# Performance work log

Measured on AMD Instinct MI355X. Metric: run time of the kernel, lower is better.

## Reference

```python
import jax, jax.numpy as jnp
import numpy as np

B, S, H, T, DI, HID, K, HEADS = 8, 1024, 768, 8, 64, 128, 8, 2
NEG = 1.0e12


def _build_adj(spans):
    # spans: [K,3] int; returns [K+1,K+1] edge multiplicity matrix (dst, src)
    s, e = spans[:, 0], spans[:, 1]
    same = (s[:, None] == s[None, :]) & (e[:, None] == e[None, :])
    # contain[i,j]: span i strictly contains span j (source appends this edge twice)
    contain = (s[:, None] <= s[None, :]) & (e[None, :] <= e[:, None]) & (~same)
    N = K + 1
    adj = jnp.eye(N, dtype=jnp.float32)                    # PyG add_self_loops
    adj = adj.at[1:, 0].add(1.0)                           # global -> span i
    adj = adj.at[0, 1:].add(1.0)                           # span i -> global
    adj = adj.at[1:, 1:].add(2.0 * contain.T.astype(jnp.float32))
    return adj


def _gat(x, adj, W, a_src, a_dst, b):
    # x [N,F]; adj [N,N] multiplicity with layout (dst, src). PyG GATConv math.
    N = x.shape[0]
    h = (x @ W).reshape(N, HEADS, -1)                      # [N,Hd,D]
    asrc = jnp.einsum('nhd,hd->nh', h, a_src)
    adst = jnp.einsum('nhd,hd->nh', h, a_dst)
    ee = jax.nn.leaky_relu(adst[:, None, :] + asrc[None, :, :], 0.2)  # [dst,src,Hd]
    logmult = jnp.where(adj > 0, jnp.log(jnp.maximum(adj, 1e-20)), 0.0)
    scores = jnp.where(adj[:, :, None] > 0, ee + logmult[:, :, None], -1e30)
    attn = jax.nn.softmax(scores, axis=1)                  # softmax over source nodes
    out = jnp.einsum('dsh,shf->dhf', attn, h).reshape(N, -1)
    return out + b


def _layernorm(x, g, bta):
    mu = x.mean(-1, keepdims=True)
    var = x.var(-1, keepdims=True)
    return (x - mu) / jnp.sqrt(var + 1e-5) * g + bta


def _forward(hidden, attention_mask, spans, W1, a_src1, a_dst1, b1, ln_g, ln_b,
             W2, a_src2, a_dst2, b2, dense_W, dense_b,
             g_centers, g_sigmas, g_weights, corr):
    start, end, etype = spans[..., 0], spans[..., 1], spans[..., 2]  # [B,K]
    pos = jnp.arange(S)
    span_mask = ((pos[None, None, :] >= start[..., None]) &
                 (pos[None, None, :] <= end[..., None])).astype(hidden.dtype)  # [B,K,S]
    span_len = (end - start + 1).astype(hidden.dtype)
    span_feat = jnp.einsum('bks,bsh->bkh', span_mask, hidden) / span_len[..., None]
    global_feat = hidden.mean(axis=1, keepdims=True)                 # [B,1,H]
    nodes = jnp.concatenate([global_feat, span_feat], axis=1)        # [B,K+1,H]
    adj = jax.vmap(_build_adj)(spans)                                # [B,K+1,K+1]

    g1 = jax.vmap(lambda x, a: _gat(x, a, W1, a_src1, a_dst1, b1))(nodes, adj)
    g1 = _layernorm(jax.nn.relu(g1), ln_g, ln_b)
    g2 = jax.vmap(lambda x, a: _gat(x, a, W2, a_src2, a_dst2, b2))(g1, adj)
    g2 = jax.nn.relu(g2)
    enhanced = g2.mean(axis=1)                                       # per-graph mean pool [B,2*HID]

    cover = span_mask.sum(axis=1)                                    # [B,S] how many spans cover token s
    token_enh = cover[..., None] * enhanced[:, None, :]              # [B,S,2*HID]
    combined = jnp.concatenate([hidden, token_enh], axis=-1)

    qk = (combined @ dense_W + dense_b).reshape(B, S, T, 2 * DI)
    qw, kw = qk[..., :DI], qk[..., DI:]

    # RoPE (sin/cos interleaved exactly as in source)
    inv = jnp.power(10000.0, -2.0 * jnp.arange(DI // 2) / DI)
    ang = pos[:, None].astype(jnp.float32) * inv[None, :]            # [S,DI/2]
    sin = jnp.repeat(jnp.sin(ang), 2, axis=-1)[None, :, None, :]     # [1,S,1,DI]
    cos = jnp.repeat(jnp.cos(ang), 2, axis=-1)[None, :, None, :]

    def rot(v):
        v2 = jnp.stack([-v[..., 1::2], v[..., ::2]], axis=-1).reshape(v.shape)
        return v * cos + v2 * sin

    qw, kw = rot(qw), rot(kw)

    logits = jnp.einsum('bmtd,bntd->btmn', qw, kw)                   # [B,T,S,S]

    # multi-modal gaussian kernel span maps (vectorized over batch/span/component)
    pf = pos.astype(jnp.float32)
    dxs = pf[None, None, None, :] - start[..., None, None] - g_centers[None, None, :, None]
    dxe = pf[None, None, None, :] - end[..., None, None] - g_centers[None, None, :, None]
    Ksr = g_weights[None, None, :, None] * jnp.exp(-0.5 * (dxs / g_sigmas[None, None, :, None]) ** 2)
    Ken = g_weights[None, None, :, None] * jnp.exp(-0.5 * (dxe / g_sigmas[None, None, :, None]) ** 2)
    gmap = jnp.einsum('bkcm,bkcn->bkmn', Ksr, Ken)                   # [B,K,S,S]
    corr_span = corr[etype]                                          # [B,K,T]
    logits = logits + jnp.einsum('bkt,bkmn->btmn', corr_span, gmap)

    pad = attention_mask[:, None, None, :]                           # key-dim-only mask (as in source)
    logits = logits * pad - (1.0 - pad) * NEG
    tril = jnp.tril(jnp.ones((S, S), logits.dtype), -1)
    logits = logits - tril * NEG
    return logits / jnp.sqrt(jnp.float32(DI))


def setup_inputs() -> dict:
    key = jax.random.key(0)
    ks = jax.random.split(key, 16)
    hidden = jax.random.normal(ks[0], (B, S, H), jnp.float32)
    attention_mask = jnp.ones((B, S), jnp.float32)
    start = jax.random.randint(ks[1], (B, K), 0, S - 32)
    length = jax.random.randint(ks[2], (B, K), 1, 16)
    spans = jnp.stack([start, start + length,
                       jax.random.randint(ks[3], (B, K), 0, T)], axis=-1).astype(jnp.int32)
    sd = 0.05
    return {
        'hidden': hidden,
        'attention_mask': attention_mask,
        'spans': spans,
        'W1': jax.random.normal(ks[4], (H, HEADS * HID), jnp.float32) * sd,
        'a_src1': jax.random.normal(ks[5], (HEADS, HID), jnp.float32) * sd,
        'a_dst1': jax.random.normal(ks[6], (HEADS, HID), jnp.float32) * sd,
        'b1': jnp.zeros((HEADS * HID,), jnp.float32),
        'ln_g': jnp.ones((HEADS * HID,), jnp.float32),
        'ln_b': jnp.zeros((HEADS * HID,), jnp.float32),
        'W2': jax.random.normal(ks[7], (HEADS * HID, HEADS * HID), jnp.float32) * sd,
        'a_src2': jax.random.normal(ks[8], (HEADS, HID), jnp.float32) * sd,
        'a_dst2': jax.random.normal(ks[9], (HEADS, HID), jnp.float32) * sd,
        'b2': jnp.zeros((HEADS * HID,), jnp.float32),
        'dense_W': jax.random.normal(ks[10], (H + HEADS * HID, T * 2 * DI), jnp.float32) * sd,
        'dense_b': jnp.zeros((T * 2 * DI,), jnp.float32),
        'g_centers': jnp.array([0.0, 0.0], jnp.float32),
        'g_sigmas': jnp.array([1.0, 3.0], jnp.float32),
        'g_weights': jnp.array([0.5, 0.5], jnp.float32),
        'corr': jnp.eye(T, dtype=jnp.float32),
    }


def reference(hidden, attention_mask, spans, W1, a_src1, a_dst1, b1, ln_g, ln_b,
              W2, a_src2, a_dst2, b2, dense_W, dense_b,
              g_centers, g_sigmas, g_weights, corr):
    return _forward(hidden, attention_mask, spans, W1, a_src1, a_dst1, b1, ln_g, ln_b,
                    W2, a_src2, a_dst2, b2, dense_W, dense_b,
                    g_centers, g_sigmas, g_weights, corr)
```

## Files before the change

### kernel.cpp

```cpp
#include <hip/hip_runtime.h>
#include <cstdint>
#include <cstddef>

#define BB 8
#define SS 1024
#define HH 768
#define TT 8
#define DII 64
#define HIDD 128
#define KSP 8
#define NHEADS 2
#define NNODES 9
#define GDIM 256
#define CDIM 1024
#define DAUGP 96
#define NEGV 1e12f

using bf16x8 = __attribute__((ext_vector_type(8))) __bf16;
using f32x4  = __attribute__((ext_vector_type(4))) float;

static __device__ inline unsigned short f2bf(float x) {
  union { float f; unsigned u; } v; v.f = x;
  unsigned r = v.u + 0x7fff + ((v.u >> 16) & 1);
  return (unsigned short)(r >> 16);
}

__global__ void kc1_cvt_hidden(const float* __restrict__ hidden, unsigned short* __restrict__ hbf) {
  int idx = blockIdx.x * 256 + threadIdx.x;
  float4 v = *(const float4*)(hidden + (size_t)idx * 4);
  ushort4 o; o.x = f2bf(v.x); o.y = f2bf(v.y); o.z = f2bf(v.z); o.w = f2bf(v.w);
  *(ushort4*)(hbf + (size_t)idx * 4) = o;
}

__global__ void kc2_cvt_wtop(const float* __restrict__ dense_W, unsigned short* __restrict__ WtopT) {
  __shared__ float t[32][33];
  int k0 = blockIdx.x * 32, n0 = blockIdx.y * 32;
  int tid = threadIdx.x;
  int r = tid >> 3, c4 = (tid & 7) * 4;
  float4 v = *(const float4*)&dense_W[(size_t)(k0 + r) * CDIM + n0 + c4];
  t[r][c4 + 0] = v.x; t[r][c4 + 1] = v.y; t[r][c4 + 2] = v.z; t[r][c4 + 3] = v.w;
  __syncthreads();
  int ro = tid >> 3, co4 = (tid & 7) * 4;
  ushort4 o;
  o.x = f2bf(t[co4 + 0][ro]); o.y = f2bf(t[co4 + 1][ro]);
  o.z = f2bf(t[co4 + 2][ro]); o.w = f2bf(t[co4 + 3][ro]);
  *(ushort4*)&WtopT[(size_t)(n0 + ro) * HH + k0 + co4] = o;
}

__global__ void k1a_spans(const float* __restrict__ hidden, const int* __restrict__ spans,
                          float* __restrict__ nodes, float* __restrict__ cover) {
  int b = blockIdx.x, tid = threadIdx.x;
  __shared__ int sp[KSP * 3];
  if (tid < KSP * 3) sp[tid] = spans[b * KSP * 3 + tid];
  __syncthreads();
  for (int s = tid; s < SS; s += 256) {
    float c = 0.f;
    #pragma unroll
    for (int k = 0; k < KSP; k++)
      c += (s >= sp[k * 3] && s <= sp[k * 3 + 1]) ? 1.f : 0.f;
    cover[b * SS + s] = c;
  }
  const float* hb = hidden + (size_t)b * SS * HH;
  for (int k = 0; k < KSP; k++) {
    int st = sp[k * 3], en = sp[k * 3 + 1];
    float inv = 1.f / (float)(en - st + 1);
    #pragma unroll
    for (int ci = 0; ci < 3; ci++) {
      int c = tid + ci * 256;
      float a = 0.f;
      #pragma unroll
      for (int j = 0; j < 16; j++) {
        int s = st + j;
        int sc = (s <= en) ? s : en;
        float v = hb[(size_t)sc * HH + c];
        a += (s <= en) ? v : 0.f;
      }
      nodes[((size_t)b * NNODES + (k + 1)) * HH + c] = a * inv;
    }
  }
}

__global__ void k1b_partial(const float* __restrict__ hidden, float* __restrict__ part) {
  int z = blockIdx.x, b = blockIdx.y, tid = threadIdx.x;
  const float* hb = hidden + (size_t)b * SS * HH;
  #pragma unroll
  for (int j = 0; j < 3; j++) {
    int c = tid + j * 256;
    float acc = 0.f;
    #pragma unroll 8
    for (int r = z * 64; r < z * 64 + 64; r++) acc += hb[(size_t)r * HH + c];
    part[((size_t)b * 16 + z) * HH + c] = acc;
  }
}
__global__ void k1c_reduce(const float* __restrict__ part, float* __restrict__ nodes) {
  int b = blockIdx.x, tid = threadIdx.x;
  #pragma unroll
  for (int j = 0; j < 3; j++) {
    int c = tid + j * 256;
    float s = 0.f;
    #pragma unroll
    for (int z = 0; z < 16; z++) s += part[((size_t)b * 16 + z) * HH + c];
    nodes[(size_t)b * NNODES * HH + c] = s / (float)SS;
  }
}

__global__ __launch_bounds__(256) void k2_gat(
    const float* __restrict__ nodes_g, const int* __restrict__ spans,
    const float* __restrict__ W1, const float* __restrict__ a_src1,
    const float* __restrict__ a_dst1, const float* __restrict__ b1,
    const float* __restrict__ ln_g, const float* __restrict__ ln_b,
    const float* __restrict__ W2, const float* __restrict__ a_src2,
    const float* __restrict__ a_dst2, const float* __restrict__ b2,
    float* __restrict__ enhg) {
  int b = blockIdx.x, tid = threadIdx.x;
  __shared__ __align__(16) float nod[NNODES * HH];
  __shared__ __align__(16) float hbuf[NNODES * GDIM];
  __shared__ __align__(16) float gbuf[NNODES * GDIM];
  __shared__ float asrc[NNODES * NHEADS], adst[NNODES * NHEADS];
  __shared__ float adjm[NNODES * NNODES];
  __shared__ float attn[NNODES * NNODES * NHEADS];
  __shared__ float mu_s[NNODES], rs_s[NNODES];
  __shared__ int sp[KSP * 3];
  if (tid < KSP * 3) sp[tid] = spans[b * KSP * 3 + tid];
  for (int i = tid; i < NNODES * HH; i += 256)
    nod[i] = nodes_g[(size_t)b * NNODES * HH + i];
  __syncthreads();
  {
    float acc[NNODES];
    #pragma unroll
    for (int n = 0; n < NNODES; n++) acc[n] = 0.f;
    #pragma unroll 2
    for (int d0 = 0; d0 < HH; d0 += 4) {
      float4 nv[NNODES];
      #pragma unroll
      for (int n = 0; n < NNODES; n++) nv[n] = *(const float4*)&nod[n * HH + d0];
      float w0 = W1[(size_t)(d0 + 0) * GDIM + tid];
      float w1 = W1[(size_t)(d0 + 1) * GDIM + tid];
      float w2 = W1[(size_t)(d0 + 2) * GDIM + tid];
      float w3 = W1[(size_t)(d0 + 3) * GDIM + tid];
      #pragma unroll
      for (int n = 0; n < NNODES; n++)
        acc[n] += nv[n].x * w0 + nv[n].y * w1 + nv[n].z * w2 + nv[n].w * w3;
    }
    #pragma unroll
    for (int n = 0; n < NNODES; n++) hbuf[n * GDIM + tid] = acc[n];
  }
  if (tid < NNODES * NNODES) {
    int i = tid / NNODES, j = tid % NNODES;
    float a = (i == j) ? 1.f : 0.f;
    if (i > 0 && j == 0) a += 1.f;
    if (i == 0 && j > 0) a += 1.f;
    if (i > 0 && j > 0 && i != j) {
      int x = j - 1, y = i - 1;
      int sx = sp[x * 3], ex = sp[x * 3 + 1], sy = sp[y * 3], ey = sp[y * 3 + 1];
      bool same = (sx == sy) && (ex == ey);
      if (sx <= sy && ey <= ex && !same) a += 2.f;
    }
    adjm[tid] = a;
  }
  __syncthreads();
  if (tid < NNODES * NHEADS) {
    int n = tid >> 1, hd = tid & 1;
    float sa = 0.f, sd = 0.f;
    #pragma unroll 8
    for (int f = 0; f < HIDD; f++) {
      float v = hbuf[n * GDIM + hd * HIDD + f];
      sa += v * a_src1[hd * HIDD + f];
      sd += v * a_dst1[hd * HIDD + f];
    }
    asrc[tid] = sa; adst[tid] = sd;
  }
  __syncthreads();
  if (tid < NNODES * NHEADS) {
    int d = tid >> 1, hd = tid & 1;
    float sc[NNODES]; float mx = -1e30f;
    for (int s2 = 0; s2 < NNODES; s2++) {
      float a = adjm[d * NNODES + s2]; float v;
      if (a > 0.f) {
        float e = adst[d * 2 + hd] + asrc[s2 * 2 + hd];
        e = (e > 0.f) ? e : 0.2f * e;
        v = e + __logf(a);
      } else v = -1e30f;
      sc[s2] = v; mx = fmaxf(mx, v);
    }
    float ssum = 0.f;
    for (int s2 = 0; s2 < NNODES; s2++) { float ex = __expf(sc[s2] - mx); sc[s2] = ex; ssum += ex; }
    float inv = 1.f / ssum;
    for (int s2 = 0; s2 < NNODES; s2++) attn[(d * NNODES + s2) * NHEADS + hd] = sc[s2] * inv;
  }
  __syncthreads();
  {
    int hd = tid >> 7;
    float bb = b1[tid];
    for (int d = 0; d < NNODES; d++) {
      float acc = bb;
      #pragma unroll
      for (int s2 = 0; s2 < NNODES; s2++)
        acc += attn[(d * NNODES + s2) * NHEADS + hd] * hbuf[s2 * GDIM + tid];
      gbuf[d * GDIM + tid] = fmaxf(acc, 0.f);
    }
  }
  __syncthreads();
  if (tid < NNODES) {
    float s1 = 0.f, s2v = 0.f;
    #pragma unroll 8
    for (int o = 0; o < GDIM; o++) { float v = gbuf[tid * GDIM + o]; s1 += v; s2v += v * v; }
    float mu = s1 / (float)GDIM;
    float var = s2v / (float)GDIM - mu * mu;
    mu_s[tid] = mu; rs_s[tid] = rsqrtf(var + 1e-5f);
  }
  __syncthreads();
  {
    float g = ln_g[tid], bt = ln_b[tid];
    for (int d = 0; d < NNODES; d++)
      gbuf[d * GDIM + tid] = (gbuf[d * GDIM + tid] - mu_s[d]) * rs_s[d] * g + bt;
  }
  __syncthreads();
  {
    float acc[NNODES];
    #pragma unroll
    for (int n = 0; n < NNODES; n++) acc[n] = 0.f;
    #pragma unroll 2
    for (int d0 = 0; d0 < GDIM; d0 += 4) {
      float4 nv[NNODES];
      #pragma unroll
      for (int n = 0; n < NNODES; n++) nv[n] = *(const float4*)&gbuf[n * GDIM + d0];
      float w0 = W2[(size_t)(d0 + 0) * GDIM + tid];
      float w1 = W2[(size_t)(d0 + 1) * GDIM + tid];
      float w2 = W2[(size_t)(d0 + 2) * GDIM + tid];
      float w3 = W2[(size_t)(d0 + 3) * GDIM + tid];
      #pragma unroll
      for (int n = 0; n < NNODES; n++)
        acc[n] += nv[n].x * w0 + nv[n].y * w1 + nv[n].z * w2 + nv[n].w * w3;
    }
    #pragma unroll
    for (int n = 0; n < NNODES; n++) hbuf[n * GDIM + tid] = acc[n];
  }
  __syncthreads();
  if (tid < NNODES * NHEADS) {
    int n = tid >> 1, hd = tid & 1;
    float sa = 0.f, sd = 0.f;
    #pragma unroll 8
    for (int f = 0; f < HIDD; f++) {
      float v = hbuf[n * GDIM + hd * HIDD + f];
      sa += v * a_src2[hd * HIDD + f];
      sd += v * a_dst2[hd * HIDD + f];
    }
    asrc[tid] = sa; adst[tid] = sd;
  }
  __syncthreads();
  if (tid < NNODES * NHEADS) {
    int d = tid >> 1, hd = tid & 1;
    float sc[NNODES]; float mx = -1e30f;
    for (int s2 = 0; s2 < NNODES; s2++) {
      float a = adjm[d * NNODES + s2]; float v;
      if (a > 0.f) {
        float e = adst[d * 2 + hd] + asrc[s2 * 2 + hd];
        e = (e > 0.f) ? e : 0.2f * e;
        v = e + __logf(a);
      } else v = -1e30f;
      sc[s2] = v; mx = fmaxf(mx, v);
    }
    float ssum = 0.f;
    for (int s2 = 0; s2 < NNODES; s2++) { float ex = __expf(sc[s2] - mx); sc[s2] = ex; ssum += ex; }
    float inv = 1.f / ssum;
    for (int s2 = 0; s2 < NNODES; s2++) attn[(d * NNODES + s2) * NHEADS + hd] = sc[s2] * inv;
  }
  __syncthreads();
  {
    int hd = tid >> 7;
    float bb = b2[tid];
    float msum = 0.f;
    for (int d = 0; d < NNODES; d++) {
      float acc = bb;
      #pragma unroll
      for (int s2 = 0; s2 < NNODES; s2++)
        acc += attn[(d * NNODES + s2) * NHEADS + hd] * hbuf[s2 * GDIM + tid];
      msum += fmaxf(acc, 0.f);
    }
    enhg[b * GDIM + tid] = msum / 9.f;
  }
}

__global__ void k2b_e2(const float* __restrict__ enhg, const float* __restrict__ dense_W,
                       float* __restrict__ E2) {
  int b = blockIdx.y, tid = threadIdx.x;
  int o = blockIdx.x * 256 + tid;
  __shared__ __align__(16) float eh[GDIM];
  eh[tid] = enhg[b * GDIM + tid];
  __syncthreads();
  float acc = 0.f;
  #pragma unroll 2
  for (int d = 0; d < GDIM; d += 4) {
    float4 ev = *(const float4*)&eh[d];
    acc += ev.x * dense_W[(size_t)(HH + d + 0) * CDIM + o];
    acc += ev.y * dense_W[(size_t)(HH + d + 1) * CDIM + o];
    acc += ev.z * dense_W[(size_t)(HH + d + 2) * CDIM + o];
    acc += ev.w * dense_W[(size_t)(HH + d + 3) * CDIM + o];
  }
  E2[b * CDIM + o] = acc;
}

__global__ __launch_bounds__(256) void k3_dense(
    const unsigned short* __restrict__ hbf, const unsigned short* __restrict__ WtopT,
    const float* __restrict__ dense_b, const float* __restrict__ cover,
    const float* __restrict__ E2, float* __restrict__ qk) {
  __shared__ unsigned short As[128 * 40];
  __shared__ unsigned short Bs[128 * 40];
  int tid = threadIdx.x;
  int n0 = blockIdx.x * 128, m0 = blockIdx.y * 128;
  int wave = tid >> 6, lane = tid & 63;
  int wr = wave >> 1, wc = wave & 1;
  int colL = lane & 15, quad = lane >> 4;
  f32x4 acc[4][4];
  #pragma unroll
  for (int i = 0; i < 4; i++)
    #pragma unroll
    for (int j = 0; j < 4; j++) { acc[i][j][0] = 0.f; acc[i][j][1] = 0.f; acc[i][j][2] = 0.f; acc[i][j][3] = 0.f; }
  for (int k0 = 0; k0 < HH; k0 += 32) {
    uint4 va[2], vb[2];
    #pragma unroll
    for (int it = 0; it < 2; it++) {
      int idx = tid + it * 256;
      int r = idx >> 2, seg = idx & 3;
      va[it] = *(const uint4*)(hbf + (size_t)(m0 + r) * HH + k0 + seg * 8);
      vb[it] = *(const uint4*)(WtopT + (size_t)(n0 + r) * HH + k0 + seg * 8);
    }
    __syncthreads();
    #pragma unroll
    for (int it = 0; it < 2; it++) {
      int idx = tid + it * 256;
      int r = idx >> 2, seg = idx & 3;
      *(uint4*)&As[r * 40 + seg * 8] = va[it];
      *(uint4*)&Bs[r * 40 + seg * 8] = vb[it];
    }
    __syncthreads();
    bf16x8 af[4], bf[4];
    #pragma unroll
    for (int tm = 0; tm < 4; tm++)
      af[tm] = *(const bf16x8*)&As[(wr * 64 + tm * 16 + colL) * 40 + quad * 8];
    #pragma unroll
    for (int tn = 0; tn < 4; tn++)
      bf[tn] = *(const bf16x8*)&Bs[(wc * 64 + tn * 16 + colL) * 40 + quad * 8];
    #pragma unroll
    for (int tm = 0; tm < 4; tm++)
      #pragma unroll
      for (int tn = 0; tn < 4; tn++)
        acc[tm][tn] = __builtin_amdgcn_mfma_f32_16x16x32_bf16(af[tm], bf[tn], acc[tm][tn], 0, 0, 0);
  }
  int b = m0 >> 10;
  #pragma unroll
  for (int tn = 0; tn < 4; tn++) {
    int col = n0 + wc * 64 + tn * 16 + colL;
    float e2 = E2[b * CDIM + col];
    float db = dense_b[col];
    #pragma unroll
    for (int tm = 0; tm < 4; tm++) {
      int rbase = m0 + wr * 64 + tm * 16 + quad * 4;
      #pragma unroll
      for (int r = 0; r < 4; r++) {
        int m = rbase + r;
        qk[(size_t)m * CDIM + col] = acc[tm][tn][r] + cover[m] * e2 + db;
      }
    }
  }
}

__global__ void k4_ropeaug(const float* __restrict__ qk, const int* __restrict__ spans,
                           const float* __restrict__ corr, const float* __restrict__ gc,
                           const float* __restrict__ gs, const float* __restrict__ gw,
                           unsigned short* __restrict__ Qa, unsigned short* __restrict__ Ka) {
  int tid = threadIdx.x;
  int g = tid >> 5, lane = tid & 31;
  int row = blockIdx.x * 8 + g;
  int b = row >> 10, s = row & 1023;
  const float* qrow = qk + (size_t)row * CDIM;
  const float LOG1E4_32 = 0.28782313662425576f;
  #pragma unroll
  for (int it = 0; it < 8; it++) {
    int cbase = it * 128 + lane * 4;
    float4 v = *(const float4*)(qrow + cbase);
    int t = cbase >> 7;
    int d = cbase & 127;
    int dd = d & 63;
    int i0 = dd >> 1;
    float inv0 = __expf(-(float)i0 * LOG1E4_32);
    float inv1 = __expf(-(float)(i0 + 1) * LOG1E4_32);
    float s0, c0, s1, c1;
    __sincosf((float)s * inv0, &s0, &c0);
    __sincosf((float)s * inv1, &s1, &c1);
    float o0 = v.x * c0 - v.y * s0;
    float o1 = v.y * c0 + v.x * s0;
    float o2 = v.z * c1 - v.w * s1;
    float o3 = v.w * c1 + v.z * s1;
    ushort4 w; w.x = f2bf(o0); w.y = f2bf(o1); w.z = f2bf(o2); w.w = f2bf(o3);
    size_t base = ((size_t)(b * TT + t) * SS + s) * DAUGP;
    if (d < 64) *(ushort4*)(Qa + base + dd) = w;
    else        *(ushort4*)(Ka + base + dd) = w;
  }
  int j = lane & 15;
  int kp = j >> 1, c = j & 1;
  int st = spans[(b * KSP + kp) * 3 + 0];
  int en = spans[(b * KSP + kp) * 3 + 1];
  int et = spans[(b * KSP + kp) * 3 + 2];
  float sig = gs[c], wgt = gw[c], ce = gc[c];
  if (lane < 16) {
    float dx = ((float)(s - st) - ce) / sig;
    float e = wgt * __expf(-0.5f * dx * dx);
    #pragma unroll
    for (int t = 0; t < TT; t++) {
      size_t base = ((size_t)(b * TT + t) * SS + s) * DAUGP;
      Qa[base + 64 + j] = f2bf(corr[et * TT + t] * e);
      Qa[base + 80 + j] = 0;
    }
  } else {
    float dx = ((float)(s - en) - ce) / sig;
    unsigned short bv = f2bf(wgt * __expf(-0.5f * dx * dx));
    #pragma unroll
    for (int t = 0; t < TT; t++) {
      size_t base = ((size_t)(b * TT + t) * SS + s) * DAUGP;
      Ka[base + 64 + j] = bv;
      Ka[base + 80 + j] = 0;
    }
  }
}

__global__ __launch_bounds__(256) void k5_logits(
    const unsigned short* __restrict__ Qa, const unsigned short* __restrict__ Ka,
    const float* __restrict__ amask, float* __restrict__ out) {
  int bz = blockIdx.z; int b = bz >> 3;
  int n0 = blockIdx.x * 128, m0 = blockIdx.y * 128;
  int tid = threadIdx.x;
  if (n0 + 127 < m0) {
    int r0 = tid >> 5, c4 = (tid & 31) * 4;
    float4 pv = *(const float4*)&amask[b * SS + n0 + c4];
    float4 o;
    o.x = (-(1.f - pv.x) * NEGV - NEGV) * 0.125f;
    o.y = (-(1.f - pv.y) * NEGV - NEGV) * 0.125f;
    o.z = (-(1.f - pv.z) * NEGV - NEGV) * 0.125f;
    o.w = (-(1.f - pv.w) * NEGV - NEGV) * 0.125f;
    for (int r = r0; r < 128; r += 8)
      *(float4*)&out[((size_t)bz * SS + m0 + r) * SS + n0 + c4] = o;
    return;
  }
  __shared__ unsigned short Qs[128 * 104];
  __shared__ unsigned short Ks[128 * 104];
  const unsigned short* Qrow = Qa + ((size_t)bz * SS + m0) * DAUGP;
  const unsigned short* Krow = Ka + ((size_t)bz * SS + n0) * DAUGP;
  #pragma unroll
  for (int it = 0; it < 6; it++) {
    int idx = tid + it * 256;
    int r = idx / 12, seg = idx % 12;
    uint4 vq = *(const uint4*)(Qrow + (size_t)r * DAUGP + seg * 8);
    uint4 vk = *(const uint4*)(Krow + (size_t)r * DAUGP + seg * 8);
    *(uint4*)&Qs[r * 104 + seg * 8] = vq;
    *(uint4*)&Ks[r * 104 + seg * 8] = vk;
  }
  __syncthreads();
  int wave = tid >> 6, lane = tid & 63;
  int wr = wave >> 1, wc = wave & 1;
  int colL = lane & 15, quad = lane >> 4;
  f32x4 acc[4][4];
  #pragma unroll
  for (int i = 0; i < 4; i++)
    #pragma unroll
    for (int j = 0; j < 4; j++) { acc[i][j][0] = 0.f; acc[i][j][1] = 0.f; acc[i][j][2] = 0.f; acc[i][j][3] = 0.f; }
  #pragma unroll
  for (int ks = 0; ks < 3; ks++) {
    bf16x8 af[4], bf[4];
    #pragma unroll
    for (int tm = 0; tm < 4; tm++)
      af[tm] = *(const bf16x8*)&Qs[(wr * 64 + tm * 16 + colL) * 104 + ks * 32 + quad * 8];
    #pragma unroll
    for (int tn = 0; tn < 4; tn++)
      bf[tn] = *(const bf16x8*)&Ks[(wc * 64 + tn * 16 + colL) * 104 + ks * 32 + quad * 8];
    #pragma unroll
    for (int tm = 0; tm < 4; tm++)
      #pragma unroll
      for (int tn = 0; tn < 4; tn++)
        acc[tm][tn] = __builtin_amdgcn_mfma_f32_16x16x32_bf16(af[tm], bf[tn], acc[tm][tn], 0, 0, 0);
  }
  #pragma unroll
  for (int tn = 0; tn < 4; tn++) {
    int col = n0 + wc * 64 + tn * 16 + colL;
    float p = amask[b * SS + col];
    float negp = -(1.f - p) * NEGV;
    #pragma unroll
    for (int tm = 0; tm < 4; tm++) {
      int rbase = m0 + wr * 64 + tm * 16 + quad * 4;
      #pragma unroll
      for (int r = 0; r < 4; r++) {
        int m = rbase + r;
        float v = acc[tm][tn][r] * p + negp;
        if (col < m) v -= NEGV;
        out[((size_t)bz * SS + m) * SS + col] = v * 0.125f;
      }
    }
  }
}

extern "C" void kernel_launch(void* const* d_in, const int* in_sizes, int n_in,
                              void* d_out, int out_size, void* d_ws, size_t ws_size,
                              hipStream_t stream) {
  const float* hidden  = (const float*)d_in[0];
  const float* amask   = (const float*)d_in[1];
  const int*   spans   = (const int*)d_in[2];
  const float* W1      = (const float*)d_in[3];
  const float* a_src1  = (const float*)d_in[4];
  const float* a_dst1  = (const float*)d_in[5];
  const float* b1      = (const float*)d_in[6];
  const float* ln_g    = (const float*)d_in[7];
  const float* ln_b    = (const float*)d_in[8];
  const float* W2      = (const float*)d_in[9];
  const float* a_src2  = (const float*)d_in[10];
  const float* a_dst2  = (const float*)d_in[11];
  const float* b2      = (const float*)d_in[12];
  const float* dense_W = (const float*)d_in[13];
  const float* dense_b = (const float*)d_in[14];
  const float* gc      = (const float*)d_in[15];
  const float* gs      = (const float*)d_in[16];
  const float* gw      = (const float*)d_in[17];
  const float* corr    = (const float*)d_in[18];

  char* wsb = (char*)d_ws;
  float* qk            = (float*)wsb;                         wsb += (size_t)BB * SS * CDIM * 4;
  unsigned short* hbf  = (unsigned short*)wsb;                wsb += (size_t)BB * SS * HH * 2;
  unsigned short* WtopT= (unsigned short*)wsb;                wsb += (size_t)CDIM * HH * 2;
  unsigned short* Qa   = (unsigned short*)wsb;                wsb += (size_t)BB * TT * SS * DAUGP * 2;
  unsigned short* Ka   = (unsigned short*)wsb;                wsb += (size_t)BB * TT * SS * DAUGP * 2;
  float* nodes         = (float*)wsb;                         wsb += (size_t)BB * NNODES * HH * 4;
  float* cover         = (float*)wsb;                         wsb += (size_t)BB * SS * 4;
  float* E2            = (float*)wsb;                         wsb += (size_t)BB * CDIM * 4;
  float* enhg          = (float*)wsb;                         wsb += (size_t)BB * GDIM * 4;
  float* part          = (float*)wsb;                         wsb += (size_t)BB * 16 * HH * 4;
  float* outp = (float*)d_out;

  kc1_cvt_hidden<<<(BB * SS * HH / 4) / 256, 256, 0, stream>>>(hidden, hbf);
  kc2_cvt_wtop<<<dim3(HH / 32, CDIM / 32), 256, 0, stream>>>(dense_W, WtopT);
  k1a_spans<<<BB, 256, 0, stream>>>(hidden, spans, nodes, cover);
  k1b_partial<<<dim3(16, BB), 256, 0, stream>>>(hidden, part);
  k1c_reduce<<<BB, 256, 0, stream>>>(part, nodes);
  k2_gat<<<BB, 256, 0, stream>>>(nodes, spans, W1, a_src1, a_dst1, b1, ln_g, ln_b,
                                 W2, a_src2, a_dst2, b2, enhg);
  k2b_e2<<<dim3(CDIM / 256, BB), 256, 0, stream>>>(enhg, dense_W, E2);
  k3_dense<<<dim3(CDIM / 128, (BB * SS) / 128), 256, 0, stream>>>(hbf, WtopT, dense_b,
                                                                  cover, E2, qk);
  k4_ropeaug<<<(BB * SS) / 8, 256, 0, stream>>>(qk, spans, corr, gc, gs, gw, Qa, Ka);
  k5_logits<<<dim3(8, 8, BB * TT), 256, 0, stream>>>(Qa, Ka, amask, outp);
}
```

Before: 598.4 us.

## Fuse RoPE into dense GEMM epilogue, merge conversion with mean partials, widen GAT

The rotary embedding is now applied in the dense GEMM epilogue, using a lane shuffle to fetch the paired element, and bf16 results are written straight into Qa/Ka. This removes the fp32 qk intermediate and its round trip through global memory. The hidden-to-bf16 conversion now also produces the partial sums for the global mean, so hidden is read once less, and the final reduce is folded into the GAT kernel. The span pooling runs on a per-span grid, and the GAT kernel uses 512 threads that split the K dimension of each matmul. Risks include scattered 2-byte epilogue stores and the extra shared-memory reduction step in the GAT kernel.

```diff
diff --git a/kernel.cpp b/kernel.cpp
--- a/kernel.cpp
+++ b/kernel.cpp
@@ -25,11 +25,24 @@
   return (unsigned short)(r >> 16);
 }
 
-__global__ void kc1_cvt_hidden(const float* __restrict__ hidden, unsigned short* __restrict__ hbf) {
-  int idx = blockIdx.x * 256 + threadIdx.x;
-  float4 v = *(const float4*)(hidden + (size_t)idx * 4);
-  ushort4 o; o.x = f2bf(v.x); o.y = f2bf(v.y); o.z = f2bf(v.z); o.w = f2bf(v.w);
-  *(ushort4*)(hbf + (size_t)idx * 4) = o;
+__global__ void kc1b_cvt_partial(const float* __restrict__ hidden,
+                                 unsigned short* __restrict__ hbf,
+                                 float* __restrict__ part) {
+  int z = blockIdx.x, b = blockIdx.y, tid = threadIdx.x;
+  const float* hb = hidden + (size_t)b * SS * HH;
+  unsigned short* ho = hbf + (size_t)b * SS * HH;
+  #pragma unroll
+  for (int j = 0; j < 3; j++) {
+    int c = tid + j * 256;
+    float acc = 0.f;
+    #pragma unroll 8
+    for (int r = z * 64; r < z * 64 + 64; r++) {
+      float v = hb[(size_t)r * HH + c];
+      ho[(size_t)r * HH + c] = f2bf(v);
+      acc += v;
+    }
+    part[((size_t)b * 16 + z) * HH + c] = acc;
+  }
 }
 
 __global__ void kc2_cvt_wtop(const float* __restrict__ dense_W, unsigned short* __restrict__ WtopT) {
@@ -49,63 +62,39 @@
 
 __global__ void k1a_spans(const float* __restrict__ hidden, const int* __restrict__ spans,
                           float* __restrict__ nodes, float* __restrict__ cover) {
-  int b = blockIdx.x, tid = threadIdx.x;
+  int k = blockIdx.x, b = blockIdx.y, tid = threadIdx.x;
   __shared__ int sp[KSP * 3];
   if (tid < KSP * 3) sp[tid] = spans[b * KSP * 3 + tid];
   __syncthreads();
-  for (int s = tid; s < SS; s += 256) {
+  if (tid < 128) {
+    int s = k * 128 + tid;
     float c = 0.f;
     #pragma unroll
-    for (int k = 0; k < KSP; k++)
-      c += (s >= sp[k * 3] && s <= sp[k * 3 + 1]) ? 1.f : 0.f;
+    for (int kk = 0; kk < KSP; kk++)
+      c += (s >= sp[kk * 3] && s <= sp[kk * 3 + 1]) ? 1.f : 0.f;
     cover[b * SS + s] = c;
   }
+  int st = sp[k * 3], en = sp[k * 3 + 1];
+  float inv = 1.f / (float)(en - st + 1);
   const float* hb = hidden + (size_t)b * SS * HH;
-  for (int k = 0; k < KSP; k++) {
-    int st = sp[k * 3], en = sp[k * 3 + 1];
-    float inv = 1.f / (float)(en - st + 1);
-    #pragma unroll
-    for (int ci = 0; ci < 3; ci++) {
-      int c = tid + ci * 256;
-      float a = 0.f;
-      #pragma unroll
-      for (int j = 0; j < 16; j++) {
-        int s = st + j;
-        int sc = (s <= en) ? s : en;
-        float v = hb[(size_t)sc * HH + c];
-        a += (s <= en) ? v : 0.f;
-      }
-      nodes[((size_t)b * NNODES + (k + 1)) * HH + c] = a * inv;
-    }
-  }
-}
-
-__global__ void k1b_partial(const float* __restrict__ hidden, float* __restrict__ part) {
-  int z = blockIdx.x, b = blockIdx.y, tid = threadIdx.x;
-  const float* hb = hidden + (size_t)b * SS * HH;
-  #pragma unroll
-  for (int j = 0; j < 3; j++) {
-    int c = tid + j * 256;
-    float acc = 0.f;
-    #pragma unroll 8
-    for (int r = z * 64; r < z * 64 + 64; r++) acc += hb[(size_t)r * HH + c];
-    part[((size_t)b * 16 + z) * HH + c] = acc;
-  }
-}
-__global__ void k1c_reduce(const float* __restrict__ part, float* __restrict__ nodes) {
-  int b = blockIdx.x, tid = threadIdx.x;
-  #pragma unroll
-  for (int j = 0; j < 3; j++) {
-    int c = tid + j * 256;
-    float s = 0.f;
-    #pragma unroll
-    for (int z = 0; z < 16; z++) s += part[((size_t)b * 16 + z) * HH + c];
-    nodes[(size_t)b * NNODES * HH + c] = s / (float)SS;
-  }
-}
-
-__global__ __launch_bounds__(256) void k2_gat(
-    const float* __restrict__ nodes_g, const int* __restrict__ spans,
+  #pragma unroll
+  for (int ci = 0; ci < 3; ci++) {
+    int c = tid + ci * 256;
+    float a = 0.f;
+    #pragma unroll
+    for (int j = 0; j < 16; j++) {
+      int s = st + j;
+      int sc = (s <= en) ? s : en;
+      float v = hb[(size_t)sc * HH + c];
+      a += (s <= en) ? v : 0.f;
+    }
+    nodes[((size_t)b * NNODES + (k + 1)) * HH + c] = a * inv;
+  }
+}
+
+__global__ __launch_bounds__(512) void k2_gat(
+    const float* __restrict__ part, const float* __restrict__ nodes_g,
+    const int* __restrict__ spans,
     const float* __restrict__ W1, const float* __restrict__ a_src1,
     const float* __restrict__ a_dst1, const float* __restrict__ b1,
     const float* __restrict__ ln_g, const float* __restrict__ ln_b,
@@ -116,37 +105,52 @@
   __shared__ __align__(16) float nod[NNODES * HH];
   __shared__ __align__(16) float hbuf[NNODES * GDIM];
   __shared__ __align__(16) float gbuf[NNODES * GDIM];
+  __shared__ __align__(16) float pbuf[2 * NNODES * GDIM];
   __shared__ float asrc[NNODES * NHEADS], adst[NNODES * NHEADS];
   __shared__ float adjm[NNODES * NNODES];
   __shared__ float attn[NNODES * NNODES * NHEADS];
   __shared__ float mu_s[NNODES], rs_s[NNODES];
   __shared__ int sp[KSP * 3];
   if (tid < KSP * 3) sp[tid] = spans[b * KSP * 3 + tid];
-  for (int i = tid; i < NNODES * HH; i += 256)
-    nod[i] = nodes_g[(size_t)b * NNODES * HH + i];
+  for (int c = tid; c < HH; c += 512) {
+    float s = 0.f;
+    #pragma unroll
+    for (int z = 0; z < 16; z++) s += part[((size_t)b * 16 + z) * HH + c];
+    nod[c] = s * (1.f / (float)SS);
+  }
+  for (int i = tid; i < (NNODES - 1) * HH; i += 512)
+    nod[HH + i] = nodes_g[(size_t)b * NNODES * HH + HH + i];
   __syncthreads();
   {
+    int col = tid & 255, h = tid >> 8;
     float acc[NNODES];
     #pragma unroll
     for (int n = 0; n < NNODES; n++) acc[n] = 0.f;
+    int dlo = h * 384;
     #pragma unroll 2
-    for (int d0 = 0; d0 < HH; d0 += 4) {
+    for (int d0 = dlo; d0 < dlo + 384; d0 += 4) {
       float4 nv[NNODES];
       #pragma unroll
       for (int n = 0; n < NNODES; n++) nv[n] = *(const float4*)&nod[n * HH + d0];
-      float w0 = W1[(size_t)(d0 + 0) * GDIM + tid];
-      float w1 = W1[(size_t)(d0 + 1) * GDIM + tid];
-      float w2 = W1[(size_t)(d0 + 2) * GDIM + tid];
-      float w3 = W1[(size_t)(d0 + 3) * GDIM + tid];
+      float w0 = W1[(size_t)(d0 + 0) * GDIM + col];
+      float w1 = W1[(size_t)(d0 + 1) * GDIM + col];
+      float w2 = W1[(size_t)(d0 + 2) * GDIM + col];
+      float w3 = W1[(size_t)(d0 + 3) * GDIM + col];
       #pragma unroll
       for (int n = 0; n < NNODES; n++)
         acc[n] += nv[n].x * w0 + nv[n].y * w1 + nv[n].z * w2 + nv[n].w * w3;
     }
     #pragma unroll
-    for (int n = 0; n < NNODES; n++) hbuf[n * GDIM + tid] = acc[n];
-  }
-  if (tid < NNODES * NNODES) {
-    int i = tid / NNODES, j = tid % NNODES;
+    for (int n = 0; n < NNODES; n++) pbuf[(h * NNODES + n) * GDIM + col] = acc[n];
+  }
+  __syncthreads();
+  if (tid < GDIM) {
+    #pragma unroll
+    for (int n = 0; n < NNODES; n++)
+      hbuf[n * GDIM + tid] = pbuf[n * GDIM + tid] + pbuf[(NNODES + n) * GDIM + tid];
+  } else if (tid < 256 + NNODES * NNODES) {
+    int q = tid - 256;
+    int i = q / NNODES, j = q % NNODES;
     float a = (i == j) ? 1.f : 0.f;
     if (i > 0 && j == 0) a += 1.f;
     if (i == 0 && j > 0) a += 1.f;
@@ -156,7 +160,7 @@
       bool same = (sx == sy) && (ex == ey);
       if (sx <= sy && ey <= ex && !same) a += 2.f;
     }
-    adjm[tid] = a;
+    adjm[q] = a;
   }
   __syncthreads();
   if (tid < NNODES * NHEADS) {
@@ -189,11 +193,11 @@
     for (int s2 = 0; s2 < NNODES; s2++) attn[(d * NNODES + s2) * NHEADS + hd] = sc[s2] * inv;
   }
   __syncthreads();
-  {
+  if (tid < 256) {
     int hd = tid >> 7;
-    float bb = b1[tid];
+    float bbv = b1[tid];
     for (int d = 0; d < NNODES; d++) {
-      float acc = bb;
+      float acc = bbv;
       #pragma unroll
       for (int s2 = 0; s2 < NNODES; s2++)
         acc += attn[(d * NNODES + s2) * NHEADS + hd] * hbuf[s2 * GDIM + tid];
@@ -210,31 +214,39 @@
     mu_s[tid] = mu; rs_s[tid] = rsqrtf(var + 1e-5f);
   }
   __syncthreads();
-  {
+  if (tid < 256) {
     float g = ln_g[tid], bt = ln_b[tid];
     for (int d = 0; d < NNODES; d++)
       gbuf[d * GDIM + tid] = (gbuf[d * GDIM + tid] - mu_s[d]) * rs_s[d] * g + bt;
   }
   __syncthreads();
   {
+    int col = tid & 255, h = tid >> 8;
     float acc[NNODES];
     #pragma unroll
     for (int n = 0; n < NNODES; n++) acc[n] = 0.f;
+    int dlo = h * 128;
     #pragma unroll 2
-    for (int d0 = 0; d0 < GDIM; d0 += 4) {
+    for (int d0 = dlo; d0 < dlo + 128; d0 += 4) {
       float4 nv[NNODES];
       #pragma unroll
       for (int n = 0; n < NNODES; n++) nv[n] = *(const float4*)&gbuf[n * GDIM + d0];
-      float w0 = W2[(size_t)(d0 + 0) * GDIM + tid];
-      float w1 = W2[(size_t)(d0 + 1) * GDIM + tid];
-      float w2 = W2[(size_t)(d0 + 2) * GDIM + tid];
-      float w3 = W2[(size_t)(d0 + 3) * GDIM + tid];
+      float w0 = W2[(size_t)(d0 + 0) * GDIM + col];
+      float w1 = W2[(size_t)(d0 + 1) * GDIM + col];
+      float w2 = W2[(size_t)(d0 + 2) * GDIM + col];
+      float w3 = W2[(size_t)(d0 + 3) * GDIM + col];
       #pragma unroll
       for (int n = 0; n < NNODES; n++)
         acc[n] += nv[n].x * w0 + nv[n].y * w1 + nv[n].z * w2 + nv[n].w * w3;
     }
     #pragma unroll
-    for (int n = 0; n < NNODES; n++) hbuf[n * GDIM + tid] = acc[n];
+    for (int n = 0; n < NNODES; n++) pbuf[(h * NNODES + n) * GDIM + col] = acc[n];
+  }
+  __syncthreads();
+  if (tid < GDIM) {
+    #pragma unroll
+    for (int n = 0; n < NNODES; n++)
+      hbuf[n * GDIM + tid] = pbuf[n * GDIM + tid] + pbuf[(NNODES + n) * GDIM + tid];
   }
   __syncthreads();
   if (tid < NNODES * NHEADS) {
@@ -267,12 +279,12 @@
     for (int s2 = 0; s2 < NNODES; s2++) attn[(d * NNODES + s2) * NHEADS + hd] = sc[s2] * inv;
   }
   __syncthreads();
-  {
+  if (tid < 256) {
     int hd = tid >> 7;
-    float bb = b2[tid];
+    float bbv = b2[tid];
     float msum = 0.f;
     for (int d = 0; d < NNODES; d++) {
-      float acc = bb;
+      float acc = bbv;
       #pragma unroll
       for (int s2 = 0; s2 < NNODES; s2++)
         acc += attn[(d * NNODES + s2) * NHEADS + hd] * hbuf[s2 * GDIM + tid];
@@ -304,7 +316,8 @@
 __global__ __launch_bounds__(256) void k3_dense(
     const unsigned short* __restrict__ hbf, const unsigned short* __restrict__ WtopT,
     const float* __restrict__ dense_b, const float* __restrict__ cover,
-    const float* __restrict__ E2, float* __restrict__ qk) {
+    const float* __restrict__ E2,
+    unsigned short* __restrict__ Qa, unsigned short* __restrict__ Ka) {
   __shared__ unsigned short As[128 * 40];
   __shared__ unsigned short Bs[128 * 40];
   int tid = threadIdx.x;
@@ -349,55 +362,45 @@
         acc[tm][tn] = __builtin_amdgcn_mfma_f32_16x16x32_bf16(af[tm], bf[tn], acc[tm][tn], 0, 0, 0);
   }
   int b = m0 >> 10;
+  const float LOG1E4_32 = 0.28782313662425576f;
+  unsigned short* __restrict__ dst = (wc == 0) ? Qa : Ka;
   #pragma unroll
   for (int tn = 0; tn < 4; tn++) {
     int col = n0 + wc * 64 + tn * 16 + colL;
     float e2 = E2[b * CDIM + col];
     float db = dense_b[col];
+    int t = col >> 7;
+    int dd = tn * 16 + colL;
+    int i0 = dd >> 1;
+    float inv = __expf(-(float)i0 * LOG1E4_32);
+    float sgn = (dd & 1) ? 1.f : -1.f;
+    size_t tbase = (size_t)(b * TT + t) * SS;
     #pragma unroll
     for (int tm = 0; tm < 4; tm++) {
       int rbase = m0 + wr * 64 + tm * 16 + quad * 4;
       #pragma unroll
       for (int r = 0; r < 4; r++) {
         int m = rbase + r;
-        qk[(size_t)m * CDIM + col] = acc[tm][tn][r] + cover[m] * e2 + db;
+        int s = m & 1023;
+        float w = acc[tm][tn][r] + cover[m] * e2 + db;
+        float p = __shfl_xor(w, 1, 64);
+        float sn, cs;
+        __sincosf((float)s * inv, &sn, &cs);
+        float o = w * cs + sgn * p * sn;
+        dst[(tbase + s) * DAUGP + dd] = f2bf(o);
       }
     }
   }
 }
 
-__global__ void k4_ropeaug(const float* __restrict__ qk, const int* __restrict__ spans,
-                           const float* __restrict__ corr, const float* __restrict__ gc,
-                           const float* __restrict__ gs, const float* __restrict__ gw,
-                           unsigned short* __restrict__ Qa, unsigned short* __restrict__ Ka) {
+__global__ void k4g_gauss(const int* __restrict__ spans, const float* __restrict__ corr,
+                          const float* __restrict__ gc, const float* __restrict__ gs,
+                          const float* __restrict__ gw,
+                          unsigned short* __restrict__ Qa, unsigned short* __restrict__ Ka) {
   int tid = threadIdx.x;
   int g = tid >> 5, lane = tid & 31;
   int row = blockIdx.x * 8 + g;
   int b = row >> 10, s = row & 1023;
-  const float* qrow = qk + (size_t)row * CDIM;
-  const float LOG1E4_32 = 0.28782313662425576f;
-  #pragma unroll
-  for (int it = 0; it < 8; it++) {
-    int cbase = it * 128 + lane * 4;
-    float4 v = *(const float4*)(qrow + cbase);
-    int t = cbase >> 7;
-    int d = cbase & 127;
-    int dd = d & 63;
-    int i0 = dd >> 1;
-    float inv0 = __expf(-(float)i0 * LOG1E4_32);
-    float inv1 = __expf(-(float)(i0 + 1) * LOG1E4_32);
-    float s0, c0, s1, c1;
-    __sincosf((float)s * inv0, &s0, &c0);
-    __sincosf((float)s * inv1, &s1, &c1);
-    float o0 = v.x * c0 - v.y * s0;
-    float o1 = v.y * c0 + v.x * s0;
-    float o2 = v.z * c1 - v.w * s1;
-    float o3 = v.w * c1 + v.z * s1;
-    ushort4 w; w.x = f2bf(o0); w.y = f2bf(o1); w.z = f2bf(o2); w.w = f2bf(o3);
-    size_t base = ((size_t)(b * TT + t) * SS + s) * DAUGP;
-    if (d < 64) *(ushort4*)(Qa + base + dd) = w;
-    else        *(ushort4*)(Ka + base + dd) = w;
-  }
   int j = lane & 15;
   int kp = j >> 1, c = j & 1;
   int st = spans[(b * KSP + kp) * 3 + 0];
@@ -523,7 +526,6 @@
   const float* corr    = (const float*)d_in[18];
 
   char* wsb = (char*)d_ws;
-  float* qk            = (float*)wsb;                         wsb += (size_t)BB * SS * CDIM * 4;
   unsigned short* hbf  = (unsigned short*)wsb;                wsb += (size_t)BB * SS * HH * 2;
   unsigned short* WtopT= (unsigned short*)wsb;                wsb += (size_t)CDIM * HH * 2;
   unsigned short* Qa   = (unsigned short*)wsb;                wsb += (size_t)BB * TT * SS * DAUGP * 2;
@@ -535,16 +537,14 @@
   float* part          = (float*)wsb;                         wsb += (size_t)BB * 16 * HH * 4;
   float* outp = (float*)d_out;
 
-  kc1_cvt_hidden<<<(BB * SS * HH / 4) / 256, 256, 0, stream>>>(hidden, hbf);
+  kc1b_cvt_partial<<<dim3(16, BB), 256, 0, stream>>>(hidden, hbf, part);
   kc2_cvt_wtop<<<dim3(HH / 32, CDIM / 32), 256, 0, stream>>>(dense_W, WtopT);
-  k1a_spans<<<BB, 256, 0, stream>>>(hidden, spans, nodes, cover);
-  k1b_partial<<<dim3(16, BB), 256, 0, stream>>>(hidden, part);
-  k1c_reduce<<<BB, 256, 0, stream>>>(part, nodes);
-  k2_gat<<<BB, 256, 0, stream>>>(nodes, spans, W1, a_src1, a_dst1, b1, ln_g, ln_b,
+  k1a_spans<<<dim3(KSP, BB), 256, 0, stream>>>(hidden, spans, nodes, cover);
+  k4g_gauss<<<(BB * SS) / 8, 256, 0, stream>>>(spans, corr, gc, gs, gw, Qa, Ka);
+  k2_gat<<<BB, 512, 0, stream>>>(part, nodes, spans, W1, a_src1, a_dst1, b1, ln_g, ln_b,
                                  W2, a_src2, a_dst2, b2, enhg);
   k2b_e2<<<dim3(CDIM / 256, BB), 256, 0, stream>>>(enhg, dense_W, E2);
   k3_dense<<<dim3(CDIM / 128, (BB * SS) / 128), 256, 0, stream>>>(hbf, WtopT, dense_b,
-                                                                  cover, E2, qk);
-  k4_ropeaug<<<(BB * SS) / 8, 256, 0, stream>>>(qk, spans, corr, gc, gs, gw, Qa, Ka);
+                                                                  cover, E2, Qa, Ka);
   k5_logits<<<dim3(8, 8, BB * TT), 256, 0, stream>>>(Qa, Ka, amask, outp);
 }
```

Measured after the change: 559.9 us. 6.4% less time.
